# Kernel tuning notes

Hardware: AMD Instinct MI355X
Metric: run time of the kernel (lower is better)

The kernel has to match this reference:

```python
import jax, jax.numpy as jnp
import numpy as np

N_QUBITS = 14
N_TROTTER = 10
EVO_TIME = 1.0
BATCH = 2048
DIM = 2 ** N_QUBITS

# (-1)**bit_q(idx) for every basis index (Qiskit little-endian: qubit q <-> bit q)
_bits = (np.arange(DIM)[:, None] >> np.arange(N_QUBITS)[None, :]) & 1
_SIGNS = np.asarray(1 - 2 * _bits, dtype=np.float32)  # (DIM, n)


def _apply_1q(psi, U, q, n):
    A = 2 ** (n - 1 - q)
    B = 2 ** q
    psi = psi.reshape(A, 2, B)
    psi = jnp.einsum('ij,ajb->aib', U, psi)
    return psi.reshape(-1)


def _apply_zz(psi, theta, q, n):
    # CX(q,q+1); RZ(theta) on q+1; CX(q,q+1)  ==  diagonal exp(-i*theta/2 * Z_q Z_{q+1})
    A = 2 ** (n - 2 - q)
    B = 2 ** q
    em = jnp.exp(-0.5j * theta)
    ep = jnp.exp(0.5j * theta)
    diag = jnp.stack([em, ep, ep, em])  # axis index = 2*bit_{q+1} + bit_q
    psi = psi.reshape(A, 4, B) * diag[None, :, None]
    return psi.reshape(-1)


def _base_state(J, g):
    # Fixed part of the circuit (same for every sample): H on all qubits, then Trotter steps.
    n = N_QUBITS
    dt = EVO_TIME / N_TROTTER
    inv = 1.0 / np.sqrt(2.0)
    H = jnp.array([[inv, inv], [inv, -inv]], dtype=jnp.complex64)
    psi = jnp.zeros(DIM, dtype=jnp.complex64).at[0].set(1.0)
    for q in range(n):
        psi = _apply_1q(psi, H, q, n)
    for _ in range(N_TROTTER):
        for i in range(n - 1):
            psi = _apply_zz(psi, J[i] * dt, i, n)
        for i in range(n):
            half = 0.5 * g[i] * dt
            c = jnp.cos(half).astype(jnp.complex64)
            ms = -1j * jnp.sin(half)
            RX = jnp.stack([jnp.stack([c, ms]), jnp.stack([ms, c])])
            psi = _apply_1q(psi, RX, i, n)
    return psi


def _expectations(psi):
    # psi: (batch, DIM). Original observable order: block i -> qubit n-1-i, [X, Y, Z].
    n = N_QUBITS
    outs = []
    for i in range(n):
        q = n - 1 - i
        A = 2 ** (n - 1 - q)
        B = 2 ** q
        pr = psi.reshape(-1, A, 2, B)
        p0 = pr[:, :, 0, :]
        p1 = pr[:, :, 1, :]
        c = jnp.sum(jnp.conj(p0) * p1, axis=(1, 2))
        outs.append(2.0 * jnp.real(c))  # <X_q>
        outs.append(2.0 * jnp.imag(c))  # <Y_q>
        outs.append(jnp.sum(p0.real ** 2 + p0.imag ** 2 - p1.real ** 2 - p1.imag ** 2, axis=(1, 2)))  # <Z_q>
    return jnp.stack(outs, axis=1).astype(jnp.float32)


def setup_inputs() -> dict:
    key = jax.random.key(0)
    kx, kj, kg = jax.random.split(key, 3)
    x = jax.random.normal(kx, (BATCH, N_QUBITS), dtype=jnp.float32)
    J = jax.random.uniform(kj, (N_QUBITS - 1,), minval=0.5, maxval=1.5, dtype=jnp.float32)
    g = jax.random.uniform(kg, (N_QUBITS,), minval=0.5, maxval=1.5, dtype=jnp.float32)
    return {"x": x, "J": J, "g": g}


def reference(x, J, g):
    psi0 = _base_state(J, g)  # (DIM,), shared across the batch
    S = jnp.asarray(_SIGNS)   # (DIM, n)
    # Final per-sample RZ(x[b,q]) on qubit q -> diagonal phase exp(-i/2 * sum_q x_q * (-1)^bit_q)
    phase = jnp.exp((-0.5j) * (x @ S.T).astype(jnp.complex64))  # (batch, DIM)
    psi = psi0[None, :] * phase
    return _expectations(psi)
```

## Files before the change

### kernel.cpp

```cpp
#include <hip/hip_runtime.h>

#define NQ     14
#define DIMQ   16384
#define NTROT  10
#define NWG    16
#define NTHR   256

struct Smem {
    float2 slab[1024];
    float2 tabLo[64];
    float2 tabHi[128];
    float  red[48];
};

__device__ __forceinline__ float2 cload2(const float2* p) {
    union { unsigned long long u; float2 f; } x;
    x.u = __hip_atomic_load((const unsigned long long*)p,
                            __ATOMIC_RELAXED, __HIP_MEMORY_SCOPE_AGENT);
    return x.f;
}
__device__ __forceinline__ void cstore2(float2* p, float2 v) {
    union { unsigned long long u; float2 f; } x;
    x.f = v;
    __hip_atomic_store((unsigned long long*)p, x.u,
                       __ATOMIC_RELAXED, __HIP_MEMORY_SCOPE_AGENT);
}
__device__ __forceinline__ float cloadf(const float* p) {
    return __hip_atomic_load(p, __ATOMIC_RELAXED, __HIP_MEMORY_SCOPE_AGENT);
}
__device__ __forceinline__ void cstoref(float* p, float v) {
    __hip_atomic_store(p, v, __ATOMIC_RELAXED, __HIP_MEMORY_SCOPE_AGENT);
}

__device__ __forceinline__ void gbar(int* flags, int w, int phase) {
    __syncthreads();
    if (threadIdx.x < 64) {
        if (threadIdx.x == 0)
            __hip_atomic_store(&flags[w], phase,
                               __ATOMIC_RELAXED, __HIP_MEMORY_SCOPE_AGENT);
        for (;;) {
            int v = phase;
            if (threadIdx.x < NWG)
                v = __hip_atomic_load(&flags[threadIdx.x],
                                      __ATOMIC_RELAXED, __HIP_MEMORY_SCOPE_AGENT);
            if (__ballot(v >= phase) == ~0ull) break;
            __builtin_amdgcn_s_sleep(1);
        }
    }
    __syncthreads();
}

__device__ __forceinline__ float2 cmulf(float2 a, float2 b) {
    return make_float2(a.x * b.x - a.y * b.y, a.x * b.y + a.y * b.x);
}
__device__ __forceinline__ void bfly(float2& p0, float2& p1, float c, float s) {
    float2 n0 = make_float2(c * p0.x + s * p1.y, c * p0.y - s * p1.x);
    float2 n1 = make_float2(c * p1.x + s * p0.y, c * p1.y - s * p0.x);
    p0 = n0; p1 = n1;
}
__device__ __forceinline__ void bfly_shfl(float2& p, int mask, float c, float s) {
    float qx = __shfl_xor(p.x, mask);
    float qy = __shfl_xor(p.y, mask);
    p = make_float2(c * p.x + s * qy, c * p.y - s * qx);
}
__device__ __forceinline__ void zz_apply(const Smem& sm, float2& a, int k) {
    int d = (k ^ (k >> 1)) & 0x1FFF;
    float2 rot = cmulf(sm.tabLo[d & 63], sm.tabHi[d >> 6]);
    a = cmulf(a, rot);
}
__device__ __forceinline__ void stage_12(float2* slab, float2 r[4], int t) {
    __syncthreads();
#pragma unroll
    for (int j = 0; j < 4; ++j) slab[(t << 2) | j] = r[j];
    __syncthreads();
#pragma unroll
    for (int j = 0; j < 4; ++j) r[j] = slab[t | (j << 8)];
}
__device__ __forceinline__ void stage_21(float2* slab, float2 r[4], int t) {
    __syncthreads();
#pragma unroll
    for (int j = 0; j < 4; ++j) slab[t | (j << 8)] = r[j];
    __syncthreads();
#pragma unroll
    for (int j = 0; j < 4; ++j) r[j] = slab[(t << 2) | j];
}

__device__ __forceinline__ void reduce_qubit(Smem& sm, int sb, int i, int t) {
    float cr = 0.f, ci = 0.f, z = 0.f;
#pragma unroll
    for (int j = 0; j < 4; ++j) {
        const int m = (t << 2) | j;
        const float2 a = sm.slab[m];
        const float n = a.x * a.x + a.y * a.y;
        if ((m >> sb) & 1) {
            z -= n;
        } else {
            z += n;
            const float2 b = sm.slab[m ^ (1 << sb)];
            cr += a.x * b.x + a.y * b.y;
            ci += a.x * b.y - a.y * b.x;
        }
    }
#pragma unroll
    for (int off = 32; off; off >>= 1) {
        cr += __shfl_down(cr, off);
        ci += __shfl_down(ci, off);
        z  += __shfl_down(z, off);
    }
    if ((t & 63) == 0) {
        atomicAdd(&sm.red[3 * i + 0], cr);
        atomicAdd(&sm.red[3 * i + 1], ci);
        atomicAdd(&sm.red[3 * i + 2], z);
    }
}

template <bool FIRST>
__device__ void phaseA(Smem& sm, float2* psi, int w, int t,
                       const float* c, const float* s) {
    float2 r[4];
    if (FIRST) {
#pragma unroll
        for (int j = 0; j < 4; ++j) r[j] = make_float2(0.0078125f, 0.0f);
    } else {
#pragma unroll
        for (int j = 0; j < 4; ++j) r[j] = cload2(&psi[(w << 10) | (t << 2) | j]);
        bfly(r[0], r[1], c[0], s[0]); bfly(r[2], r[3], c[0], s[0]);
        bfly(r[0], r[2], c[1], s[1]); bfly(r[1], r[3], c[1], s[1]);
#pragma unroll
        for (int j = 0; j < 4; ++j) bfly_shfl(r[j], 1, c[2], s[2]);
#pragma unroll
        for (int j = 0; j < 4; ++j) bfly_shfl(r[j], 2, c[3], s[3]);
    }
#pragma unroll
    for (int j = 0; j < 4; ++j) zz_apply(sm, r[j], (w << 10) | (t << 2) | j);
    bfly(r[0], r[1], c[0], s[0]); bfly(r[2], r[3], c[0], s[0]);
    bfly(r[0], r[2], c[1], s[1]); bfly(r[1], r[3], c[1], s[1]);
#pragma unroll
    for (int b = 0; b < 6; ++b) {
#pragma unroll
        for (int j = 0; j < 4; ++j) bfly_shfl(r[j], 1 << b, c[2 + b], s[2 + b]);
    }
    stage_12(sm.slab, r, t);
    bfly(r[0], r[1], c[8], s[8]); bfly(r[2], r[3], c[8], s[8]);
    bfly(r[0], r[2], c[9], s[9]); bfly(r[1], r[3], c[9], s[9]);
#pragma unroll
    for (int j = 0; j < 4; ++j) cstore2(&psi[(w << 10) | t | (j << 8)], r[j]);
}

template <bool REDUCE>
__device__ void phaseB(Smem& sm, float2* psi, int w, int t,
                       const float* c, const float* s) {
    float2 r[4];
#pragma unroll
    for (int j = 0; j < 4; ++j) r[j] = cload2(&psi[(((t << 2) | j) << 4) | w]);
#pragma unroll
    for (int j = 0; j < 4; ++j) bfly_shfl(r[j], 16, c[10], s[10]);
#pragma unroll
    for (int j = 0; j < 4; ++j) bfly_shfl(r[j], 32, c[11], s[11]);
    stage_12(sm.slab, r, t);
    bfly(r[0], r[1], c[12], s[12]); bfly(r[2], r[3], c[12], s[12]);
    bfly(r[0], r[2], c[13], s[13]); bfly(r[1], r[3], c[13], s[13]);
#pragma unroll
    for (int j = 0; j < 4; ++j) zz_apply(sm, r[j], ((t | (j << 8)) << 4) | w);
    bfly(r[0], r[1], c[12], s[12]); bfly(r[2], r[3], c[12], s[12]);
    bfly(r[0], r[2], c[13], s[13]); bfly(r[1], r[3], c[13], s[13]);
#pragma unroll
    for (int b = 0; b < 6; ++b) {
#pragma unroll
        for (int j = 0; j < 4; ++j) bfly_shfl(r[j], 1 << b, c[4 + b], s[4 + b]);
    }
    stage_21(sm.slab, r, t);
#pragma unroll
    for (int j = 0; j < 4; ++j) bfly_shfl(r[j], 16, c[10], s[10]);
#pragma unroll
    for (int j = 0; j < 4; ++j) bfly_shfl(r[j], 32, c[11], s[11]);
#pragma unroll
    for (int j = 0; j < 4; ++j) cstore2(&psi[(((t << 2) | j) << 4) | w], r[j]);

    if (REDUCE) {
#pragma unroll
        for (int j = 0; j < 4; ++j) sm.slab[(t << 2) | j] = r[j];
        __syncthreads();
#pragma unroll
        for (int q = 10; q <= 13; ++q) reduce_qubit(sm, q - 4, 13 - q, t);
    }
}

__device__ void phaseA_final(Smem& sm, const float2* psi, int w, int t,
                             const float* c, const float* s, float* partials) {
    float2 r[4];
#pragma unroll
    for (int j = 0; j < 4; ++j) r[j] = cload2(&psi[(w << 10) | (t << 2) | j]);
    bfly(r[0], r[1], c[0], s[0]); bfly(r[2], r[3], c[0], s[0]);
    bfly(r[0], r[2], c[1], s[1]); bfly(r[1], r[3], c[1], s[1]);
#pragma unroll
    for (int j = 0; j < 4; ++j) bfly_shfl(r[j], 1, c[2], s[2]);
#pragma unroll
    for (int j = 0; j < 4; ++j) bfly_shfl(r[j], 2, c[3], s[3]);
    __syncthreads();
#pragma unroll
    for (int j = 0; j < 4; ++j) sm.slab[(t << 2) | j] = r[j];
    __syncthreads();
#pragma unroll
    for (int q = 0; q <= 9; ++q) reduce_qubit(sm, q, 13 - q, t);
    __syncthreads();
    if (t < 42) cstoref(&partials[w * 48 + t], sm.red[t]);
}

extern "C" __global__ void __launch_bounds__(NTHR)
qr_all(const float* __restrict__ x, const float* __restrict__ J,
       const float* __restrict__ g, float* __restrict__ out,
       float2* __restrict__ psi, float* __restrict__ partials,
       int* __restrict__ flags) {
    __shared__ Smem sm;
    const int w = blockIdx.x;
    const int t = threadIdx.x;
    const float dt = 0.1f;

    if (t < 64) {
        float phi = 0.0f;
        for (int i = 0; i < 6; ++i) {
            const float h = 0.5f * J[i] * dt;
            phi += ((t >> i) & 1) ? h : -h;
        }
        float sn, cs; __sincosf(phi, &sn, &cs);
        sm.tabLo[t] = make_float2(cs, sn);
    } else if (t < 192) {
        const int v = t - 64;
        float phi = 0.0f;
        for (int i = 0; i < 7; ++i) {
            const float h = 0.5f * J[6 + i] * dt;
            phi += ((v >> i) & 1) ? h : -h;
        }
        float sn, cs; __sincosf(phi, &sn, &cs);
        sm.tabHi[v] = make_float2(cs, sn);
    }
    if (t < 48) sm.red[t] = 0.0f;
    float cc[NQ], ss[NQ];
#pragma unroll
    for (int i = 0; i < NQ; ++i) __sincosf(0.5f * g[i] * dt, &ss[i], &cc[i]);
    __syncthreads();

    int bar = 0;
    phaseA<true>(sm, psi, w, t, cc, ss);
    gbar(flags, w, ++bar);
    for (int sstep = 1; sstep <= 9; ++sstep) {
        if (sstep & 1) {
            if (sstep == 9) phaseB<true >(sm, psi, w, t, cc, ss);
            else            phaseB<false>(sm, psi, w, t, cc, ss);
        } else {
            phaseA<false>(sm, psi, w, t, cc, ss);
        }
        gbar(flags, w, ++bar);
    }
    phaseA_final(sm, psi, w, t, cc, ss, partials);
    gbar(flags, w, ++bar);

    if (t < 42) {
        float sum = 0.0f;
#pragma unroll
        for (int w2 = 0; w2 < NWG; ++w2) sum += cloadf(&partials[w2 * 48 + t]);
        sm.red[t] = sum;
    }
    __syncthreads();
    const int gtid = w * NTHR + t;
    for (int task = gtid; task < 2048 * NQ; task += NWG * NTHR) {
        const int b = task / NQ;
        const int i = task - b * NQ;
        const int q = 13 - i;
        const float xv = x[b * NQ + q];
        const float cr = sm.red[3 * i + 0];
        const float ci = sm.red[3 * i + 1];
        const float zz = sm.red[3 * i + 2];
        float sn, cs; __sincosf(xv, &sn, &cs);
        float* o = out + b * (3 * NQ) + 3 * i;
        o[0] = 2.0f * (cs * cr - sn * ci);
        o[1] = 2.0f * (sn * cr + cs * ci);
        o[2] = zz;
    }
}

extern "C" void kernel_launch(void* const* d_in, const int* in_sizes, int n_in,
                              void* d_out, int out_size, void* d_ws, size_t ws_size,
                              hipStream_t stream) {
    const float* x = (const float*)d_in[0];
    const float* J = (const float*)d_in[1];
    const float* g = (const float*)d_in[2];
    float* out      = (float*)d_out;
    float2* psi     = (float2*)d_ws;
    int*   flags    = (int*)((char*)d_ws + DIMQ * sizeof(float2));
    float* partials = (float*)((char*)d_ws + DIMQ * sizeof(float2) + 256);
    (void)in_sizes; (void)n_in; (void)out_size; (void)ws_size;

    hipLaunchKernelGGL(qr_all, dim3(NWG), dim3(NTHR), 0, stream,
                       x, J, g, out, psi, partials, flags);
}
```

Before: 112.3 us.

## Replicate state evolution across teams and use sc0-only cache-coherent loads

```diff
diff --git a/kernel.cpp b/kernel.cpp
--- a/kernel.cpp
+++ b/kernel.cpp
@@ -5,44 +5,115 @@
 #define NTROT  10
 #define NWG    16
 #define NTHR   256
+#define TEAM_PSI_BYTES 131072
+#define CTRL_STRIDE    3072
+#define PROBE_MAGIC    0x5A5A1234
+
+typedef float vfloat4 __attribute__((ext_vector_type(4)));
 
 struct Smem {
     float2 slab[1024];
     float2 tabLo[64];
     float2 tabHi[128];
     float  red[48];
+    int    fastmode;
 };
 
-__device__ __forceinline__ float2 cload2(const float2* p) {
-    union { unsigned long long u; float2 f; } x;
-    x.u = __hip_atomic_load((const unsigned long long*)p,
-                            __ATOMIC_RELAXED, __HIP_MEMORY_SCOPE_AGENT);
-    return x.f;
-}
-__device__ __forceinline__ void cstore2(float2* p, float2 v) {
-    union { unsigned long long u; float2 f; } x;
-    x.f = v;
-    __hip_atomic_store((unsigned long long*)p, x.u,
-                       __ATOMIC_RELAXED, __HIP_MEMORY_SCOPE_AGENT);
-}
-__device__ __forceinline__ float cloadf(const float* p) {
-    return __hip_atomic_load(p, __ATOMIC_RELAXED, __HIP_MEMORY_SCOPE_AGENT);
-}
-__device__ __forceinline__ void cstoref(float* p, float v) {
-    __hip_atomic_store(p, v, __ATOMIC_RELAXED, __HIP_MEMORY_SCOPE_AGENT);
-}
-
-__device__ __forceinline__ void gbar(int* flags, int w, int phase) {
+template <bool F>
+__device__ __forceinline__ void ld4c(const float2* p, float2 r[4]) {
+    vfloat4 a, b;
+    if constexpr (F)
+        asm volatile("global_load_dwordx4 %0, %2, off sc0\n\t"
+                     "global_load_dwordx4 %1, %2, off offset:16 sc0\n\t"
+                     "s_waitcnt vmcnt(0)"
+                     : "=&v"(a), "=&v"(b) : "v"(p) : "memory");
+    else
+        asm volatile("global_load_dwordx4 %0, %2, off sc0 sc1\n\t"
+                     "global_load_dwordx4 %1, %2, off offset:16 sc0 sc1\n\t"
+                     "s_waitcnt vmcnt(0)"
+                     : "=&v"(a), "=&v"(b) : "v"(p) : "memory");
+    r[0] = make_float2(a.x, a.y); r[1] = make_float2(a.z, a.w);
+    r[2] = make_float2(b.x, b.y); r[3] = make_float2(b.z, b.w);
+}
+__device__ __forceinline__ float2 d2f2(double d) { union { double d; float2 f; } u; u.d = d; return u.f; }
+__device__ __forceinline__ double f22d(float2 f) { union { double d; float2 f; } u; u.f = f; return u.d; }
+
+template <bool F>
+__device__ __forceinline__ void ld4s(const float2* p0, const float2* p1,
+                                     const float2* p2, const float2* p3,
+                                     float2 r[4]) {
+    double d0, d1, d2, d3;
+    if constexpr (F)
+        asm volatile("global_load_dwordx2 %0, %4, off sc0\n\t"
+                     "global_load_dwordx2 %1, %5, off sc0\n\t"
+                     "global_load_dwordx2 %2, %6, off sc0\n\t"
+                     "global_load_dwordx2 %3, %7, off sc0\n\t"
+                     "s_waitcnt vmcnt(0)"
+                     : "=&v"(d0), "=&v"(d1), "=&v"(d2), "=&v"(d3)
+                     : "v"(p0), "v"(p1), "v"(p2), "v"(p3) : "memory");
+    else
+        asm volatile("global_load_dwordx2 %0, %4, off sc0 sc1\n\t"
+                     "global_load_dwordx2 %1, %5, off sc0 sc1\n\t"
+                     "global_load_dwordx2 %2, %6, off sc0 sc1\n\t"
+                     "global_load_dwordx2 %3, %7, off sc0 sc1\n\t"
+                     "s_waitcnt vmcnt(0)"
+                     : "=&v"(d0), "=&v"(d1), "=&v"(d2), "=&v"(d3)
+                     : "v"(p0), "v"(p1), "v"(p2), "v"(p3) : "memory");
+    r[0] = d2f2(d0); r[1] = d2f2(d1); r[2] = d2f2(d2); r[3] = d2f2(d3);
+}
+template <bool F>
+__device__ __forceinline__ void st2(float2* p, float2 v) {
+    if constexpr (F)
+        asm volatile("global_store_dwordx2 %0, %1, off sc0" :: "v"(p), "v"(f22d(v)) : "memory");
+    else
+        asm volatile("global_store_dwordx2 %0, %1, off sc0 sc1" :: "v"(p), "v"(f22d(v)) : "memory");
+}
+template <bool F>
+__device__ __forceinline__ void stf(float* p, float v) {
+    if constexpr (F)
+        asm volatile("global_store_dword %0, %1, off sc0" :: "v"(p), "v"(v) : "memory");
+    else
+        asm volatile("global_store_dword %0, %1, off sc0 sc1" :: "v"(p), "v"(v) : "memory");
+}
+template <bool F>
+__device__ __forceinline__ float ldf(const float* p) {
+    float v;
+    if constexpr (F)
+        asm volatile("global_load_dword %0, %1, off sc0\n\ts_waitcnt vmcnt(0)"
+                     : "=&v"(v) : "v"(p) : "memory");
+    else
+        asm volatile("global_load_dword %0, %1, off sc0 sc1\n\ts_waitcnt vmcnt(0)"
+                     : "=&v"(v) : "v"(p) : "memory");
+    return v;
+}
+template <bool F>
+__device__ __forceinline__ void sti(int* p, int v) {
+    if constexpr (F)
+        asm volatile("global_store_dword %0, %1, off sc0" :: "v"(p), "v"(v) : "memory");
+    else
+        asm volatile("global_store_dword %0, %1, off sc0 sc1" :: "v"(p), "v"(v) : "memory");
+}
+template <bool F>
+__device__ __forceinline__ int ldi(const int* p) {
+    int v;
+    if constexpr (F)
+        asm volatile("global_load_dword %0, %1, off sc0\n\ts_waitcnt vmcnt(0)"
+                     : "=&v"(v) : "v"(p) : "memory");
+    else
+        asm volatile("global_load_dword %0, %1, off sc0 sc1\n\ts_waitcnt vmcnt(0)"
+                     : "=&v"(v) : "v"(p) : "memory");
+    return v;
+}
+
+template <bool F>
+__device__ __forceinline__ void gbar(int* flags, int rank, int phase) {
+    asm volatile("s_waitcnt vmcnt(0)" ::: "memory");
     __syncthreads();
     if (threadIdx.x < 64) {
-        if (threadIdx.x == 0)
-            __hip_atomic_store(&flags[w], phase,
-                               __ATOMIC_RELAXED, __HIP_MEMORY_SCOPE_AGENT);
+        if (threadIdx.x == 0) sti<F>(&flags[rank], phase);
         for (;;) {
             int v = phase;
-            if (threadIdx.x < NWG)
-                v = __hip_atomic_load(&flags[threadIdx.x],
-                                      __ATOMIC_RELAXED, __HIP_MEMORY_SCOPE_AGENT);
+            if (threadIdx.x < NWG) v = ldi<F>(&flags[threadIdx.x]);
             if (__ballot(v >= phase) == ~0ull) break;
             __builtin_amdgcn_s_sleep(1);
         }
@@ -84,7 +155,6 @@
 #pragma unroll
     for (int j = 0; j < 4; ++j) r[j] = slab[(t << 2) | j];
 }
-
 __device__ __forceinline__ void reduce_qubit(Smem& sm, int sb, int i, int t) {
     float cr = 0.f, ci = 0.f, z = 0.f;
 #pragma unroll
@@ -114,7 +184,7 @@
     }
 }
 
-template <bool FIRST>
+template <bool F, bool FIRST>
 __device__ void phaseA(Smem& sm, float2* psi, int w, int t,
                        const float* c, const float* s) {
     float2 r[4];
@@ -122,8 +192,7 @@
 #pragma unroll
         for (int j = 0; j < 4; ++j) r[j] = make_float2(0.0078125f, 0.0f);
     } else {
-#pragma unroll
-        for (int j = 0; j < 4; ++j) r[j] = cload2(&psi[(w << 10) | (t << 2) | j]);
+        ld4c<F>(&psi[(w << 10) | (t << 2)], r);
         bfly(r[0], r[1], c[0], s[0]); bfly(r[2], r[3], c[0], s[0]);
         bfly(r[0], r[2], c[1], s[1]); bfly(r[1], r[3], c[1], s[1]);
 #pragma unroll
@@ -144,15 +213,15 @@
     bfly(r[0], r[1], c[8], s[8]); bfly(r[2], r[3], c[8], s[8]);
     bfly(r[0], r[2], c[9], s[9]); bfly(r[1], r[3], c[9], s[9]);
 #pragma unroll
-    for (int j = 0; j < 4; ++j) cstore2(&psi[(w << 10) | t | (j << 8)], r[j]);
-}
-
-template <bool REDUCE>
+    for (int j = 0; j < 4; ++j) st2<F>(&psi[(w << 10) | t | (j << 8)], r[j]);
+}
+
+template <bool F, bool REDUCE>
 __device__ void phaseB(Smem& sm, float2* psi, int w, int t,
                        const float* c, const float* s) {
     float2 r[4];
-#pragma unroll
-    for (int j = 0; j < 4; ++j) r[j] = cload2(&psi[(((t << 2) | j) << 4) | w]);
+    ld4s<F>(&psi[((t << 2) << 4) | w],       &psi[(((t << 2) | 1) << 4) | w],
+            &psi[(((t << 2) | 2) << 4) | w], &psi[(((t << 2) | 3) << 4) | w], r);
 #pragma unroll
     for (int j = 0; j < 4; ++j) bfly_shfl(r[j], 16, c[10], s[10]);
 #pragma unroll
@@ -175,7 +244,7 @@
 #pragma unroll
     for (int j = 0; j < 4; ++j) bfly_shfl(r[j], 32, c[11], s[11]);
 #pragma unroll
-    for (int j = 0; j < 4; ++j) cstore2(&psi[(((t << 2) | j) << 4) | w], r[j]);
+    for (int j = 0; j < 4; ++j) st2<F>(&psi[(((t << 2) | j) << 4) | w], r[j]);
 
     if (REDUCE) {
 #pragma unroll
@@ -186,11 +255,11 @@
     }
 }
 
+template <bool F>
 __device__ void phaseA_final(Smem& sm, const float2* psi, int w, int t,
-                             const float* c, const float* s, float* partials) {
+                             const float* c, const float* s, float* P) {
     float2 r[4];
-#pragma unroll
-    for (int j = 0; j < 4; ++j) r[j] = cload2(&psi[(w << 10) | (t << 2) | j]);
+    ld4c<F>(&psi[(w << 10) | (t << 2)], r);
     bfly(r[0], r[1], c[0], s[0]); bfly(r[2], r[3], c[0], s[0]);
     bfly(r[0], r[2], c[1], s[1]); bfly(r[1], r[3], c[1], s[1]);
 #pragma unroll
@@ -204,69 +273,45 @@
 #pragma unroll
     for (int q = 0; q <= 9; ++q) reduce_qubit(sm, q, 13 - q, t);
     __syncthreads();
-    if (t < 42) cstoref(&partials[w * 48 + t], sm.red[t]);
-}
-
-extern "C" __global__ void __launch_bounds__(NTHR)
-qr_all(const float* __restrict__ x, const float* __restrict__ J,
-       const float* __restrict__ g, float* __restrict__ out,
-       float2* __restrict__ psi, float* __restrict__ partials,
-       int* __restrict__ flags) {
-    __shared__ Smem sm;
-    const int w = blockIdx.x;
-    const int t = threadIdx.x;
-    const float dt = 0.1f;
-
-    if (t < 64) {
-        float phi = 0.0f;
-        for (int i = 0; i < 6; ++i) {
-            const float h = 0.5f * J[i] * dt;
-            phi += ((t >> i) & 1) ? h : -h;
-        }
-        float sn, cs; __sincosf(phi, &sn, &cs);
-        sm.tabLo[t] = make_float2(cs, sn);
-    } else if (t < 192) {
-        const int v = t - 64;
-        float phi = 0.0f;
-        for (int i = 0; i < 7; ++i) {
-            const float h = 0.5f * J[6 + i] * dt;
-            phi += ((v >> i) & 1) ? h : -h;
-        }
-        float sn, cs; __sincosf(phi, &sn, &cs);
-        sm.tabHi[v] = make_float2(cs, sn);
-    }
-    if (t < 48) sm.red[t] = 0.0f;
-    float cc[NQ], ss[NQ];
-#pragma unroll
-    for (int i = 0; i < NQ; ++i) __sincosf(0.5f * g[i] * dt, &ss[i], &cc[i]);
-    __syncthreads();
-
+    if (t < 42) stf<F>(&P[t * NWG + w], sm.red[t]);
+}
+
+template <bool F>
+__device__ void qr_main(Smem& sm, const float* x, float* out, float2* psi,
+                        int* flags, float* P, int rank, int t,
+                        const float* cc, const float* ss,
+                        int row0, int rows) {
     int bar = 0;
-    phaseA<true>(sm, psi, w, t, cc, ss);
-    gbar(flags, w, ++bar);
+    phaseA<F, true>(sm, psi, rank, t, cc, ss);
+    gbar<F>(flags, rank, ++bar);
     for (int sstep = 1; sstep <= 9; ++sstep) {
         if (sstep & 1) {
-            if (sstep == 9) phaseB<true >(sm, psi, w, t, cc, ss);
-            else            phaseB<false>(sm, psi, w, t, cc, ss);
+            if (sstep == 9) phaseB<F, true >(sm, psi, rank, t, cc, ss);
+            else            phaseB<F, false>(sm, psi, rank, t, cc, ss);
         } else {
-            phaseA<false>(sm, psi, w, t, cc, ss);
-        }
-        gbar(flags, w, ++bar);
-    }
-    phaseA_final(sm, psi, w, t, cc, ss, partials);
-    gbar(flags, w, ++bar);
-
+            phaseA<F, false>(sm, psi, rank, t, cc, ss);
+        }
+        gbar<F>(flags, rank, ++bar);
+    }
+    phaseA_final<F>(sm, psi, rank, t, cc, ss, P);
+    gbar<F>(flags, rank, ++bar);
+
+    float* sumbuf = (float*)sm.slab;
+    for (int idx = t; idx < 42 * NWG; idx += NTHR) sumbuf[idx] = ldf<F>(&P[idx]);
+    __syncthreads();
+    float cv = 0.0f;
     if (t < 42) {
-        float sum = 0.0f;
-#pragma unroll
-        for (int w2 = 0; w2 < NWG; ++w2) sum += cloadf(&partials[w2 * 48 + t]);
-        sm.red[t] = sum;
-    }
-    __syncthreads();
-    const int gtid = w * NTHR + t;
-    for (int task = gtid; task < 2048 * NQ; task += NWG * NTHR) {
-        const int b = task / NQ;
-        const int i = task - b * NQ;
+#pragma unroll
+        for (int k = 0; k < NWG; ++k) cv += sumbuf[t * NWG + k];
+    }
+    __syncthreads();
+    if (t < 42) sm.red[t] = cv;
+    __syncthreads();
+
+    const int ntask = rows * NQ;
+    for (int task = rank * NTHR + t; task < ntask; task += NWG * NTHR) {
+        const int b = row0 + task / NQ;
+        const int i = task - (task / NQ) * NQ;
         const int q = 13 - i;
         const float xv = x[b * NQ + q];
         const float cr = sm.red[3 * i + 0];
@@ -280,18 +325,99 @@
     }
 }
 
+extern "C" __global__ void __launch_bounds__(NTHR)
+qr_all(const float* __restrict__ x, const float* __restrict__ J,
+       const float* __restrict__ g, float* __restrict__ out,
+       char* __restrict__ ws, char* __restrict__ ctrlbase, int tshift) {
+    __shared__ Smem sm;
+    const int t = threadIdx.x;
+    const int nteams = 1 << tshift;
+    const int team = blockIdx.x & (nteams - 1);
+    const int rank = blockIdx.x >> tshift;
+    const float dt = 0.1f;
+
+    float2* psi = (float2*)(ws + (size_t)team * TEAM_PSI_BYTES);
+    char* tc   = ctrlbase + team * CTRL_STRIDE;
+    int* flags = (int*)tc;
+    int* probe = (int*)(tc + 64);
+    int* c1    = (int*)(tc + 128);
+    int* c2    = (int*)(tc + 132);
+    int* go    = (int*)(tc + 136);
+    int* fail  = (int*)(tc + 140);
+    float* P   = (float*)(tc + 192);
+
+    if (t == 255) {
+        (void)ldi<true>(probe);
+        __hip_atomic_fetch_add(c1, 1, __ATOMIC_RELAXED, __HIP_MEMORY_SCOPE_AGENT);
+        while (__hip_atomic_load(c1, __ATOMIC_RELAXED, __HIP_MEMORY_SCOPE_AGENT) < NWG)
+            __builtin_amdgcn_s_sleep(1);
+        if (rank == 0) {
+            sti<true>(probe, PROBE_MAGIC);
+            asm volatile("s_waitcnt vmcnt(0)" ::: "memory");
+            __hip_atomic_store(go, 1, __ATOMIC_RELAXED, __HIP_MEMORY_SCOPE_AGENT);
+        } else {
+            while (__hip_atomic_load(go, __ATOMIC_RELAXED, __HIP_MEMORY_SCOPE_AGENT) == 0)
+                __builtin_amdgcn_s_sleep(1);
+        }
+        if (ldi<true>(probe) != PROBE_MAGIC)
+            __hip_atomic_store(fail, 1, __ATOMIC_RELAXED, __HIP_MEMORY_SCOPE_AGENT);
+        __hip_atomic_fetch_add(c2, 1, __ATOMIC_RELAXED, __HIP_MEMORY_SCOPE_AGENT);
+        while (__hip_atomic_load(c2, __ATOMIC_RELAXED, __HIP_MEMORY_SCOPE_AGENT) < NWG)
+            __builtin_amdgcn_s_sleep(1);
+        sm.fastmode =
+            (__hip_atomic_load(fail, __ATOMIC_RELAXED, __HIP_MEMORY_SCOPE_AGENT) == 0);
+    }
+
+    if (t < 64) {
+        float phi = 0.0f;
+        for (int i = 0; i < 6; ++i) {
+            const float h = 0.5f * J[i] * dt;
+            phi += ((t >> i) & 1) ? h : -h;
+        }
+        float sn, cs; __sincosf(phi, &sn, &cs);
+        sm.tabLo[t] = make_float2(cs, sn);
+    } else if (t < 192) {
+        const int v = t - 64;
+        float phi = 0.0f;
+        for (int i = 0; i < 7; ++i) {
+            const float h = 0.5f * J[6 + i] * dt;
+            phi += ((v >> i) & 1) ? h : -h;
+        }
+        float sn, cs; __sincosf(phi, &sn, &cs);
+        sm.tabHi[v] = make_float2(cs, sn);
+    }
+    if (t < 48) sm.red[t] = 0.0f;
+    float cc[NQ], ss[NQ];
+#pragma unroll
+    for (int i = 0; i < NQ; ++i) __sincosf(0.5f * g[i] * dt, &ss[i], &cc[i]);
+    __syncthreads();
+
+    const int rows = 2048 >> tshift;
+    const int row0 = team * rows;
+    if (sm.fastmode)
+        qr_main<true >(sm, x, out, psi, flags, P, rank, t, cc, ss, row0, rows);
+    else
+        qr_main<false>(sm, x, out, psi, flags, P, rank, t, cc, ss, row0, rows);
+}
+
 extern "C" void kernel_launch(void* const* d_in, const int* in_sizes, int n_in,
                               void* d_out, int out_size, void* d_ws, size_t ws_size,
                               hipStream_t stream) {
     const float* x = (const float*)d_in[0];
     const float* J = (const float*)d_in[1];
     const float* g = (const float*)d_in[2];
-    float* out      = (float*)d_out;
-    float2* psi     = (float2*)d_ws;
-    int*   flags    = (int*)((char*)d_ws + DIMQ * sizeof(float2));
-    float* partials = (float*)((char*)d_ws + DIMQ * sizeof(float2) + 256);
-    (void)in_sizes; (void)n_in; (void)out_size; (void)ws_size;
-
-    hipLaunchKernelGGL(qr_all, dim3(NWG), dim3(NTHR), 0, stream,
-                       x, J, g, out, psi, partials, flags);
-}
+    float* out = (float*)d_out;
+    char* ws   = (char*)d_ws;
+    (void)in_sizes; (void)n_in; (void)out_size;
+
+    int tshift = 3;
+    while (tshift > 0 &&
+           ((size_t)(1 << tshift)) * (TEAM_PSI_BYTES + CTRL_STRIDE) > ws_size)
+        --tshift;
+    const int nteams = 1 << tshift;
+    char* ctrlbase = ws + (size_t)nteams * TEAM_PSI_BYTES;
+
+    hipMemsetAsync(ctrlbase, 0, (size_t)nteams * CTRL_STRIDE, stream);
+    hipLaunchKernelGGL(qr_all, dim3(nteams * NWG), dim3(NTHR), 0, stream,
+                       x, J, g, out, ws, ctrlbase, tshift);
+}
```

Result: slower. 116.8 us (+4.0%).

## Vectorize coherent global state access and remap phase B layout to cut butterflies

Applied to the files above, without the earlier changes.

```diff
diff --git a/kernel.cpp b/kernel.cpp
--- a/kernel.cpp
+++ b/kernel.cpp
@@ -5,6 +5,8 @@
 #define NTROT  10
 #define NWG    16
 #define NTHR   256
+
+typedef float vfloat4 __attribute__((ext_vector_type(4)));
 
 struct Smem {
     float2 slab[1024];
@@ -13,36 +15,57 @@
     float  red[48];
 };
 
-__device__ __forceinline__ float2 cload2(const float2* p) {
-    union { unsigned long long u; float2 f; } x;
-    x.u = __hip_atomic_load((const unsigned long long*)p,
-                            __ATOMIC_RELAXED, __HIP_MEMORY_SCOPE_AGENT);
-    return x.f;
-}
-__device__ __forceinline__ void cstore2(float2* p, float2 v) {
-    union { unsigned long long u; float2 f; } x;
-    x.f = v;
-    __hip_atomic_store((unsigned long long*)p, x.u,
-                       __ATOMIC_RELAXED, __HIP_MEMORY_SCOPE_AGENT);
-}
-__device__ __forceinline__ float cloadf(const float* p) {
-    return __hip_atomic_load(p, __ATOMIC_RELAXED, __HIP_MEMORY_SCOPE_AGENT);
-}
-__device__ __forceinline__ void cstoref(float* p, float v) {
-    __hip_atomic_store(p, v, __ATOMIC_RELAXED, __HIP_MEMORY_SCOPE_AGENT);
+__device__ __forceinline__ float2 d2f2(double d) { union { double d; float2 f; } u; u.d = d; return u.f; }
+__device__ __forceinline__ double f22d(float2 f) { union { double d; float2 f; } u; u.f = f; return u.d; }
+
+__device__ __forceinline__ void ld4c(const float2* p, float2 r[4]) {
+    vfloat4 a, b;
+    asm volatile("global_load_dwordx4 %0, %2, off sc0 sc1\n\t"
+                 "global_load_dwordx4 %1, %2, off offset:16 sc0 sc1\n\t"
+                 "s_waitcnt vmcnt(0)"
+                 : "=&v"(a), "=&v"(b) : "v"(p) : "memory");
+    r[0] = make_float2(a.x, a.y); r[1] = make_float2(a.z, a.w);
+    r[2] = make_float2(b.x, b.y); r[3] = make_float2(b.z, b.w);
+}
+__device__ __forceinline__ void st4c(float2* p, const float2 r[4]) {
+    vfloat4 a, b;
+    a.x = r[0].x; a.y = r[0].y; a.z = r[1].x; a.w = r[1].y;
+    b.x = r[2].x; b.y = r[2].y; b.z = r[3].x; b.w = r[3].y;
+    asm volatile("global_store_dwordx4 %0, %1, off sc0 sc1\n\t"
+                 "global_store_dwordx4 %0, %2, off offset:16 sc0 sc1"
+                 : : "v"(p), "v"(a), "v"(b) : "memory");
+}
+__device__ __forceinline__ void st2(float2* p, float2 v) {
+    asm volatile("global_store_dwordx2 %0, %1, off sc0 sc1"
+                 : : "v"(p), "v"(f22d(v)) : "memory");
+}
+__device__ __forceinline__ void stf(float* p, float v) {
+    asm volatile("global_store_dword %0, %1, off sc0 sc1" : : "v"(p), "v"(v) : "memory");
+}
+__device__ __forceinline__ float ldf(const float* p) {
+    float v;
+    asm volatile("global_load_dword %0, %1, off sc0 sc1\n\ts_waitcnt vmcnt(0)"
+                 : "=&v"(v) : "v"(p) : "memory");
+    return v;
+}
+__device__ __forceinline__ void sti(int* p, int v) {
+    asm volatile("global_store_dword %0, %1, off sc0 sc1" : : "v"(p), "v"(v) : "memory");
+}
+__device__ __forceinline__ int ldi(const int* p) {
+    int v;
+    asm volatile("global_load_dword %0, %1, off sc0 sc1\n\ts_waitcnt vmcnt(0)"
+                 : "=&v"(v) : "v"(p) : "memory");
+    return v;
 }
 
 __device__ __forceinline__ void gbar(int* flags, int w, int phase) {
+    asm volatile("s_waitcnt vmcnt(0)" ::: "memory");
     __syncthreads();
     if (threadIdx.x < 64) {
-        if (threadIdx.x == 0)
-            __hip_atomic_store(&flags[w], phase,
-                               __ATOMIC_RELAXED, __HIP_MEMORY_SCOPE_AGENT);
+        if (threadIdx.x == 0) sti(&flags[w], phase);
         for (;;) {
             int v = phase;
-            if (threadIdx.x < NWG)
-                v = __hip_atomic_load(&flags[threadIdx.x],
-                                      __ATOMIC_RELAXED, __HIP_MEMORY_SCOPE_AGENT);
+            if (threadIdx.x < NWG) v = ldi(&flags[threadIdx.x]);
             if (__ballot(v >= phase) == ~0ull) break;
             __builtin_amdgcn_s_sleep(1);
         }
@@ -84,7 +107,6 @@
 #pragma unroll
     for (int j = 0; j < 4; ++j) r[j] = slab[(t << 2) | j];
 }
-
 __device__ __forceinline__ void reduce_qubit(Smem& sm, int sb, int i, int t) {
     float cr = 0.f, ci = 0.f, z = 0.f;
 #pragma unroll
@@ -122,14 +144,12 @@
 #pragma unroll
         for (int j = 0; j < 4; ++j) r[j] = make_float2(0.0078125f, 0.0f);
     } else {
-#pragma unroll
-        for (int j = 0; j < 4; ++j) r[j] = cload2(&psi[(w << 10) | (t << 2) | j]);
-        bfly(r[0], r[1], c[0], s[0]); bfly(r[2], r[3], c[0], s[0]);
-        bfly(r[0], r[2], c[1], s[1]); bfly(r[1], r[3], c[1], s[1]);
-#pragma unroll
-        for (int j = 0; j < 4; ++j) bfly_shfl(r[j], 1, c[2], s[2]);
-#pragma unroll
-        for (int j = 0; j < 4; ++j) bfly_shfl(r[j], 2, c[3], s[3]);
+        ld4c(&psi[(w << 10) | (t << 2)], r);
+#pragma unroll
+        for (int b = 2; b < 6; ++b) {
+#pragma unroll
+            for (int j = 0; j < 4; ++j) bfly_shfl(r[j], 1 << b, c[2 + b], s[2 + b]);
+        }
     }
 #pragma unroll
     for (int j = 0; j < 4; ++j) zz_apply(sm, r[j], (w << 10) | (t << 2) | j);
@@ -144,15 +164,15 @@
     bfly(r[0], r[1], c[8], s[8]); bfly(r[2], r[3], c[8], s[8]);
     bfly(r[0], r[2], c[9], s[9]); bfly(r[1], r[3], c[9], s[9]);
 #pragma unroll
-    for (int j = 0; j < 4; ++j) cstore2(&psi[(w << 10) | t | (j << 8)], r[j]);
+    for (int j = 0; j < 4; ++j) st2(&psi[(w << 10) | t | (j << 8)], r[j]);
 }
 
 template <bool REDUCE>
 __device__ void phaseB(Smem& sm, float2* psi, int w, int t,
                        const float* c, const float* s) {
     float2 r[4];
-#pragma unroll
-    for (int j = 0; j < 4; ++j) r[j] = cload2(&psi[(((t << 2) | j) << 4) | w]);
+    const int kbase = ((t >> 2) << 8) | (w << 4) | ((t & 3) << 2);
+    ld4c(&psi[kbase], r);
 #pragma unroll
     for (int j = 0; j < 4; ++j) bfly_shfl(r[j], 16, c[10], s[10]);
 #pragma unroll
@@ -161,56 +181,62 @@
     bfly(r[0], r[1], c[12], s[12]); bfly(r[2], r[3], c[12], s[12]);
     bfly(r[0], r[2], c[13], s[13]); bfly(r[1], r[3], c[13], s[13]);
 #pragma unroll
-    for (int j = 0; j < 4; ++j) zz_apply(sm, r[j], ((t | (j << 8)) << 4) | w);
+    for (int j = 0; j < 4; ++j) {
+        const int m = t | (j << 8);
+        zz_apply(sm, r[j], ((m >> 4) << 8) | (w << 4) | (m & 15));
+    }
     bfly(r[0], r[1], c[12], s[12]); bfly(r[2], r[3], c[12], s[12]);
     bfly(r[0], r[2], c[13], s[13]); bfly(r[1], r[3], c[13], s[13]);
 #pragma unroll
-    for (int b = 0; b < 6; ++b) {
-#pragma unroll
-        for (int j = 0; j < 4; ++j) bfly_shfl(r[j], 1 << b, c[4 + b], s[4 + b]);
-    }
+    for (int b = 0; b < 4; ++b) {
+#pragma unroll
+        for (int j = 0; j < 4; ++j) bfly_shfl(r[j], 1 << b, c[b], s[b]);
+    }
+#pragma unroll
+    for (int j = 0; j < 4; ++j) bfly_shfl(r[j], 16, c[8], s[8]);
+#pragma unroll
+    for (int j = 0; j < 4; ++j) bfly_shfl(r[j], 32, c[9], s[9]);
     stage_21(sm.slab, r, t);
 #pragma unroll
     for (int j = 0; j < 4; ++j) bfly_shfl(r[j], 16, c[10], s[10]);
 #pragma unroll
     for (int j = 0; j < 4; ++j) bfly_shfl(r[j], 32, c[11], s[11]);
-#pragma unroll
-    for (int j = 0; j < 4; ++j) cstore2(&psi[(((t << 2) | j) << 4) | w], r[j]);
+    st4c(&psi[kbase], r);
 
     if (REDUCE) {
 #pragma unroll
         for (int j = 0; j < 4; ++j) sm.slab[(t << 2) | j] = r[j];
         __syncthreads();
 #pragma unroll
-        for (int q = 10; q <= 13; ++q) reduce_qubit(sm, q - 4, 13 - q, t);
+        for (int q = 0; q <= 3; ++q) reduce_qubit(sm, q, 13 - q, t);
+#pragma unroll
+        for (int q = 8; q <= 13; ++q) reduce_qubit(sm, q - 4, 13 - q, t);
     }
 }
 
 __device__ void phaseA_final(Smem& sm, const float2* psi, int w, int t,
-                             const float* c, const float* s, float* partials) {
+                             const float* c, const float* s, float* P) {
     float2 r[4];
-#pragma unroll
-    for (int j = 0; j < 4; ++j) r[j] = cload2(&psi[(w << 10) | (t << 2) | j]);
-    bfly(r[0], r[1], c[0], s[0]); bfly(r[2], r[3], c[0], s[0]);
-    bfly(r[0], r[2], c[1], s[1]); bfly(r[1], r[3], c[1], s[1]);
-#pragma unroll
-    for (int j = 0; j < 4; ++j) bfly_shfl(r[j], 1, c[2], s[2]);
-#pragma unroll
-    for (int j = 0; j < 4; ++j) bfly_shfl(r[j], 2, c[3], s[3]);
+    ld4c(&psi[(w << 10) | (t << 2)], r);
+#pragma unroll
+    for (int b = 2; b < 6; ++b) {
+#pragma unroll
+        for (int j = 0; j < 4; ++j) bfly_shfl(r[j], 1 << b, c[2 + b], s[2 + b]);
+    }
     __syncthreads();
 #pragma unroll
     for (int j = 0; j < 4; ++j) sm.slab[(t << 2) | j] = r[j];
     __syncthreads();
 #pragma unroll
-    for (int q = 0; q <= 9; ++q) reduce_qubit(sm, q, 13 - q, t);
-    __syncthreads();
-    if (t < 42) cstoref(&partials[w * 48 + t], sm.red[t]);
+    for (int q = 4; q <= 7; ++q) reduce_qubit(sm, q, 13 - q, t);
+    __syncthreads();
+    if (t < 42) stf(&P[t * NWG + w], sm.red[t]);
 }
 
 extern "C" __global__ void __launch_bounds__(NTHR)
 qr_all(const float* __restrict__ x, const float* __restrict__ J,
        const float* __restrict__ g, float* __restrict__ out,
-       float2* __restrict__ psi, float* __restrict__ partials,
+       float2* __restrict__ psi, float* __restrict__ P,
        int* __restrict__ flags) {
     __shared__ Smem sm;
     const int w = blockIdx.x;
@@ -253,18 +279,22 @@
         }
         gbar(flags, w, ++bar);
     }
-    phaseA_final(sm, psi, w, t, cc, ss, partials);
+    phaseA_final(sm, psi, w, t, cc, ss, P);
     gbar(flags, w, ++bar);
 
+    float* sumbuf = (float*)sm.slab;
+    for (int idx = t; idx < 42 * NWG; idx += NTHR) sumbuf[idx] = ldf(&P[idx]);
+    __syncthreads();
+    float cv = 0.0f;
     if (t < 42) {
-        float sum = 0.0f;
-#pragma unroll
-        for (int w2 = 0; w2 < NWG; ++w2) sum += cloadf(&partials[w2 * 48 + t]);
-        sm.red[t] = sum;
-    }
-    __syncthreads();
-    const int gtid = w * NTHR + t;
-    for (int task = gtid; task < 2048 * NQ; task += NWG * NTHR) {
+#pragma unroll
+        for (int k = 0; k < NWG; ++k) cv += sumbuf[t * NWG + k];
+    }
+    __syncthreads();
+    if (t < 42) sm.red[t] = cv;
+    __syncthreads();
+
+    for (int task = w * NTHR + t; task < 2048 * NQ; task += NWG * NTHR) {
         const int b = task / NQ;
         const int i = task - b * NQ;
         const int q = 13 - i;
@@ -286,12 +316,13 @@
     const float* x = (const float*)d_in[0];
     const float* J = (const float*)d_in[1];
     const float* g = (const float*)d_in[2];
-    float* out      = (float*)d_out;
-    float2* psi     = (float2*)d_ws;
-    int*   flags    = (int*)((char*)d_ws + DIMQ * sizeof(float2));
-    float* partials = (float*)((char*)d_ws + DIMQ * sizeof(float2) + 256);
+    float* out = (float*)d_out;
+    char* ws   = (char*)d_ws;
+    float2* psi  = (float2*)ws;
+    int*    flags = (int*)(ws + DIMQ * sizeof(float2));
+    float*  P     = (float*)(ws + DIMQ * sizeof(float2) + 256);
     (void)in_sizes; (void)n_in; (void)out_size; (void)ws_size;
 
     hipLaunchKernelGGL(qr_all, dim3(NWG), dim3(NTHR), 0, stream,
-                       x, J, g, out, psi, partials, flags);
-}
+                       x, J, g, out, psi, P, flags);
+}
```

Result: faster. 106.3 us (-5.4%).
